# Optimization experiments

Measured on AMD Instinct MI355X. Metric: run time of the kernel, lower is better.

The kernel has to match this reference:

```python
import math
import jax, jax.numpy as jnp
import numpy as np

B, T, N = 64, 100, 20
NR = N * (N - 1)
D_STATE, D_SHAPE, D_REL = 8, 4, 3
THRESH = 0.35


def _pair_indices(n):
    # (i, j) pairs with i != j, ordered so that relation index
    # r = i*(n-1) + j - (j > i) equals the flattened position.
    ii, jj = np.meshgrid(np.arange(n), np.arange(n), indexing='ij')
    m = ii != jj
    return ii[m], jj[m]  # each [n*(n-1)]


def setup_inputs() -> dict:
    key = jax.random.key(0)
    k1, k2, k3 = jax.random.split(key, 3)
    objects_state = jax.random.uniform(k1, (B, T, N, D_STATE), dtype=jnp.float32)
    objects_shape = jax.random.normal(k2, (B, T, N, D_SHAPE), dtype=jnp.float32)
    relation_info = jax.random.normal(k3, (B, T, NR, D_REL), dtype=jnp.float32)
    return {"objects_state": objects_state, "objects_shape": objects_shape,
            "relation_info": relation_info}


def reference(objects_state, objects_shape, relation_info):
    dt = objects_state.dtype
    i_idx, j_idx = _pair_indices(N)

    # cdist over xy positions, then threshold (diagonal is exactly 0 -> excluded by nonzero)
    pos = objects_state[..., 0:2]                                   # [B,T,N,2]
    d = jnp.linalg.norm(pos[..., :, None, :] - pos[..., None, :, :], axis=-1)  # [B,T,N,N]
    adj = (d < THRESH) & (d > 0)
    mask = adj[..., i_idx, j_idx].astype(dt)                        # [B,T,NR]

    eye = jnp.eye(N, dtype=dt)
    receiver_relations = mask[..., None] * eye[i_idx]               # [B,T,NR,N]
    sender_relations = mask[..., None] * eye[j_idx]                 # [B,T,NR,N]

    # identity scaler
    data_state, data_shape = objects_state, objects_shape

    senders_state = jnp.einsum('btrn,btnd->btrd', sender_relations, data_state)
    receivers_state = jnp.einsum('btrn,btnd->btrd', receiver_relations, data_state)
    senders_shape = jnp.einsum('btrn,btnd->btrd', sender_relations, data_shape)
    receivers_shape = jnp.einsum('btrn,btnd->btrd', receiver_relations, data_shape)

    recv_ang = receivers_state[..., 2:3]                            # [B,T,NR,1]
    half_pi = jnp.asarray(math.pi / 2, dtype=dt)
    b1 = jnp.concatenate([jnp.cos(recv_ang), jnp.sin(recv_ang)], axis=-1)
    b2 = jnp.concatenate([jnp.cos(recv_ang + half_pi), jnp.sin(recv_ang + half_pi)], axis=-1)
    basis = jnp.stack([b1, b2], axis=-2)                            # [B,T,NR,2,2]

    diff_state = senders_state - receivers_state
    diff_pos = diff_state[..., 0:2]
    diff_vel = diff_state[..., 3:5]
    control = senders_state[..., 6:8]
    angle_diff = diff_state[..., 2:3]
    angle_diff_vel = diff_state[..., 5:6]

    temp = jnp.stack([diff_pos, diff_vel, control], axis=-1)        # [B,T,NR,2,3]
    tfed = jnp.einsum('btrij,btrjk->btrik', basis, temp)            # [B,T,NR,2,3]
    diff_pos, diff_vel, control = tfed[..., 0], tfed[..., 1], tfed[..., 2]

    diff_angle_2d = jnp.concatenate([jnp.sin(2 * angle_diff), jnp.cos(2 * angle_diff)], axis=-1)
    diff_state = jnp.concatenate([diff_pos, diff_vel, control, diff_angle_2d, angle_diff_vel], axis=-1)
    rel_data = jnp.concatenate([relation_info, diff_state, receivers_shape, senders_shape], axis=-1)

    obj_ang = data_state[..., 2:3]                                  # [B,T,N,1]
    ob1 = jnp.concatenate([jnp.cos(obj_ang), jnp.sin(obj_ang)], axis=-1)
    ob2 = jnp.concatenate([jnp.cos(obj_ang + half_pi), jnp.sin(obj_ang + half_pi)], axis=-1)
    object_basis = jnp.stack([ob1, ob2], axis=-2)                   # [B,T,N,2,2]
    obj_vel = data_state[..., 3:5]
    obj_vel_tfed = jnp.einsum('btnij,btnj->btni', object_basis, obj_vel)
    obj_data = jnp.concatenate([obj_vel_tfed, data_state[..., 5:6], data_shape], axis=-1)

    return rel_data, obj_data, receiver_relations, sender_relations
```

## Files before the change

### kernel.cpp

```cpp
#include <hip/hip_runtime.h>
#include <math.h>

#define BB 64
#define TT 100
#define NN 20
#define NRR 380

typedef float f32x4 __attribute__((ext_vector_type(4)));

__global__ __launch_bounds__(256) void onehot_kernel(
    const float* __restrict__ state,
    float* __restrict__ out)
{
    const int bt  = blockIdx.x;
    const int tid = threadIdx.x;

    __shared__ float s_pos[NN * 2];
    __shared__ float s_mask[NRR];
    __shared__ int   s_ij[NRR];

    if (tid < NN * 2) {
        const int n = tid >> 1, c = tid & 1;
        s_pos[tid] = state[(size_t)bt * NN * 8 + n * 8 + c];
    }
    __syncthreads();

    const float THRESH = 0.35f;
    for (int r = tid; r < NRR; r += 256) {
        const int i = r / 19;
        const int l = r - i * 19;
        const int j = (l < i) ? l : (l + 1);
        const float dx = s_pos[i * 2 + 0] - s_pos[j * 2 + 0];
        const float dy = s_pos[i * 2 + 1] - s_pos[j * 2 + 1];
        const float d  = sqrtf(dx * dx + dy * dy);
        s_mask[r] = (d < THRESH && d > 0.0f) ? 1.0f : 0.0f;
        s_ij[r]   = i | (j << 8);
    }
    __syncthreads();

    const size_t REL_SZ = (size_t)BB * TT * NRR * 20;
    const size_t OBJ_SZ = (size_t)BB * TT * NN * 7;
    f32x4* recvb = (f32x4*)(out + REL_SZ + OBJ_SZ)          + (size_t)bt * (NRR * 5);
    f32x4* sendb = (f32x4*)(out + REL_SZ + OBJ_SZ + REL_SZ) + (size_t)bt * (NRR * 5);

#pragma unroll
    for (int k = 0; k < 8; ++k) {
        const int idx = tid + k * 256;
        if (idx < NRR * 5) {
            const int r  = idx / 5;
            const int qb = (idx - r * 5) * 4;
            const float m = s_mask[r];
            const int   i = s_ij[r] & 255;
            f32x4 rv;
            rv.x = (i == qb + 0) ? m : 0.0f;
            rv.y = (i == qb + 1) ? m : 0.0f;
            rv.z = (i == qb + 2) ? m : 0.0f;
            rv.w = (i == qb + 3) ? m : 0.0f;
            __builtin_nontemporal_store(rv, &recvb[idx]);
        }
    }
#pragma unroll
    for (int k = 0; k < 8; ++k) {
        const int idx = tid + k * 256;
        if (idx < NRR * 5) {
            const int r  = idx / 5;
            const int qb = (idx - r * 5) * 4;
            const float m = s_mask[r];
            const int   j = s_ij[r] >> 8;
            f32x4 sv;
            sv.x = (j == qb + 0) ? m : 0.0f;
            sv.y = (j == qb + 1) ? m : 0.0f;
            sv.z = (j == qb + 2) ? m : 0.0f;
            sv.w = (j == qb + 3) ? m : 0.0f;
            __builtin_nontemporal_store(sv, &sendb[idx]);
        }
    }
}

__global__ __launch_bounds__(256) void reldata_kernel(
    const float* __restrict__ state,
    const float* __restrict__ shape,
    const float* __restrict__ relinfo,
    float* __restrict__ out)
{
    const int bt  = blockIdx.x;
    const int tid = threadIdx.x;

    __shared__ float  s_state[NN * 8];
    __shared__ float  s_shape[NN * 4];
    __shared__ float4 s_row4[NRR * 5];

    const float THRESH  = 0.35f;
    const float HALF_PI = 1.57079632679489661923f;

    const int   r2v = tid + 256;
    const int   r2c = (r2v < NRR) ? r2v : (NRR - 1);
    const float* rbase = relinfo + (size_t)bt * NRR * 3;
    const float ra0 = rbase[tid * 3 + 0];
    const float ra1 = rbase[tid * 3 + 1];
    const float ra2 = rbase[tid * 3 + 2];
    const float rb0 = rbase[r2c * 3 + 0];
    const float rb1 = rbase[r2c * 3 + 1];
    const float rb2 = rbase[r2c * 3 + 2];

    if (tid < NN * 8)                   s_state[tid]          = state[(size_t)bt * NN * 8 + tid];
    else if (tid < NN * 8 + NN * 4)     s_shape[tid - NN * 8] = shape[(size_t)bt * NN * 4 + (tid - NN * 8)];
    __syncthreads();

    const size_t REL_SZ = (size_t)BB * TT * NRR * 20;
    f32x4* relb = (f32x4*)out + (size_t)bt * (NRR * 5);
    float* objb = out + REL_SZ + (size_t)bt * (NN * 7);

    if (tid < NN * 7) {
        const int n = tid / 7;
        const int c = tid - n * 7;
        float v;
        if (c < 2) {
            const float ang = s_state[n * 8 + 2];
            const float a   = (c == 0) ? ang : (ang + HALF_PI);
            v = cosf(a) * s_state[n * 8 + 3] + sinf(a) * s_state[n * 8 + 4];
        } else if (c == 2) {
            v = s_state[n * 8 + 5];
        } else {
            v = s_shape[n * 4 + (c - 3)];
        }
        objb[tid] = v;
    }

    for (int pass = 0; pass < 2; ++pass) {
        const int r = (pass == 0) ? tid : r2v;
        if (r < NRR) {
            const float f0 = (pass == 0) ? ra0 : rb0;
            const float f1 = (pass == 0) ? ra1 : rb1;
            const float f2 = (pass == 0) ? ra2 : rb2;

            const int i = r / 19;
            const int l = r - i * 19;
            const int j = (l < i) ? l : (l + 1);

            const float* si = &s_state[i * 8];
            const float* sj = &s_state[j * 8];

            const float dx = si[0] - sj[0];
            const float dy = si[1] - sj[1];
            const float d  = sqrtf(dx * dx + dy * dy);
            const float mask = (d < THRESH && d > 0.0f) ? 1.0f : 0.0f;

            const float dpx   = mask * (sj[0] - si[0]);
            const float dpy   = mask * (sj[1] - si[1]);
            const float adiff = mask * (sj[2] - si[2]);
            const float dvx   = mask * (sj[3] - si[3]);
            const float dvy   = mask * (sj[4] - si[4]);
            const float adv   = mask * (sj[5] - si[5]);
            const float cx    = mask * sj[6];
            const float cy    = mask * sj[7];

            const float rang = mask * si[2];
            const float c1 = cosf(rang),           s1 = sinf(rang);
            const float c2 = cosf(rang + HALF_PI), s2 = sinf(rang + HALF_PI);

            float4 w0, w1, w2, w3, w4;
            w0.x = f0; w0.y = f1; w0.z = f2;
            w0.w = c1 * dpx + s1 * dpy;
            w1.x = c2 * dpx + s2 * dpy;
            w1.y = c1 * dvx + s1 * dvy;
            w1.z = c2 * dvx + s2 * dvy;
            w1.w = c1 * cx  + s1 * cy;
            w2.x = c2 * cx  + s2 * cy;
            w2.y = sinf(2.0f * adiff);
            w2.z = cosf(2.0f * adiff);
            w2.w = adv;
            w3.x = mask * s_shape[i * 4 + 0];
            w3.y = mask * s_shape[i * 4 + 1];
            w3.z = mask * s_shape[i * 4 + 2];
            w3.w = mask * s_shape[i * 4 + 3];
            w4.x = mask * s_shape[j * 4 + 0];
            w4.y = mask * s_shape[j * 4 + 1];
            w4.z = mask * s_shape[j * 4 + 2];
            w4.w = mask * s_shape[j * 4 + 3];

            float4* row = &s_row4[r * 5];
            row[0] = w0; row[1] = w1; row[2] = w2; row[3] = w3; row[4] = w4;
        }
    }
    __syncthreads();

#pragma unroll
    for (int k = 0; k < 8; ++k) {
        const int idx = tid + k * 256;
        if (idx < NRR * 5) {
            const float4 w = s_row4[idx];
            f32x4 wv;
            wv.x = w.x; wv.y = w.y; wv.z = w.z; wv.w = w.w;
            __builtin_nontemporal_store(wv, &relb[idx]);
        }
    }
}

extern "C" void kernel_launch(void* const* d_in, const int* in_sizes, int n_in,
                              void* d_out, int out_size, void* d_ws, size_t ws_size,
                              hipStream_t stream) {
    const float* state = (const float*)d_in[0];
    const float* shp   = (const float*)d_in[1];
    const float* rel   = (const float*)d_in[2];
    float* out = (float*)d_out;
    reldata_kernel<<<dim3(BB * TT), dim3(256), 0, stream>>>(state, shp, rel, out);
    onehot_kernel <<<dim3(BB * TT), dim3(256), 0, stream>>>(state, out);
}
```

Measured before the change: 120.7 us.

## Fuse reldata and one-hot kernels into one role-split launch with regular stores

Merges the two kernels into a single launch of 3x blocks. Each block takes one of three roles: rel/obj data, receiver one-hot, or sender one-hot. This removes one kernel launch and the serialization between the two kernels, and splits the one-hot writes across twice as many blocks. It also replaces nontemporal stores with ordinary stores, which changes cache behaviour on a write-bound kernel. The shared memory footprint per block grows because all roles declare the union of buffers, which may lower occupancy for the lighter roles.

```diff
diff --git a/kernel.cpp b/kernel.cpp
--- a/kernel.cpp
+++ b/kernel.cpp
@@ -5,194 +5,172 @@
 #define TT 100
 #define NN 20
 #define NRR 380
+#define NBT (BB * TT)
 
 typedef float f32x4 __attribute__((ext_vector_type(4)));
 
-__global__ __launch_bounds__(256) void onehot_kernel(
-    const float* __restrict__ state,
-    float* __restrict__ out)
-{
-    const int bt  = blockIdx.x;
-    const int tid = threadIdx.x;
-
-    __shared__ float s_pos[NN * 2];
-    __shared__ float s_mask[NRR];
-    __shared__ int   s_ij[NRR];
-
-    if (tid < NN * 2) {
-        const int n = tid >> 1, c = tid & 1;
-        s_pos[tid] = state[(size_t)bt * NN * 8 + n * 8 + c];
-    }
-    __syncthreads();
-
-    const float THRESH = 0.35f;
-    for (int r = tid; r < NRR; r += 256) {
-        const int i = r / 19;
-        const int l = r - i * 19;
-        const int j = (l < i) ? l : (l + 1);
-        const float dx = s_pos[i * 2 + 0] - s_pos[j * 2 + 0];
-        const float dy = s_pos[i * 2 + 1] - s_pos[j * 2 + 1];
-        const float d  = sqrtf(dx * dx + dy * dy);
-        s_mask[r] = (d < THRESH && d > 0.0f) ? 1.0f : 0.0f;
-        s_ij[r]   = i | (j << 8);
-    }
-    __syncthreads();
-
-    const size_t REL_SZ = (size_t)BB * TT * NRR * 20;
-    const size_t OBJ_SZ = (size_t)BB * TT * NN * 7;
-    f32x4* recvb = (f32x4*)(out + REL_SZ + OBJ_SZ)          + (size_t)bt * (NRR * 5);
-    f32x4* sendb = (f32x4*)(out + REL_SZ + OBJ_SZ + REL_SZ) + (size_t)bt * (NRR * 5);
-
-#pragma unroll
-    for (int k = 0; k < 8; ++k) {
-        const int idx = tid + k * 256;
-        if (idx < NRR * 5) {
-            const int r  = idx / 5;
-            const int qb = (idx - r * 5) * 4;
-            const float m = s_mask[r];
-            const int   i = s_ij[r] & 255;
-            f32x4 rv;
-            rv.x = (i == qb + 0) ? m : 0.0f;
-            rv.y = (i == qb + 1) ? m : 0.0f;
-            rv.z = (i == qb + 2) ? m : 0.0f;
-            rv.w = (i == qb + 3) ? m : 0.0f;
-            __builtin_nontemporal_store(rv, &recvb[idx]);
-        }
-    }
-#pragma unroll
-    for (int k = 0; k < 8; ++k) {
-        const int idx = tid + k * 256;
-        if (idx < NRR * 5) {
-            const int r  = idx / 5;
-            const int qb = (idx - r * 5) * 4;
-            const float m = s_mask[r];
-            const int   j = s_ij[r] >> 8;
-            f32x4 sv;
-            sv.x = (j == qb + 0) ? m : 0.0f;
-            sv.y = (j == qb + 1) ? m : 0.0f;
-            sv.z = (j == qb + 2) ? m : 0.0f;
-            sv.w = (j == qb + 3) ? m : 0.0f;
-            __builtin_nontemporal_store(sv, &sendb[idx]);
-        }
-    }
-}
-
-__global__ __launch_bounds__(256) void reldata_kernel(
+__global__ __launch_bounds__(256) void fused_kernel(
     const float* __restrict__ state,
     const float* __restrict__ shape,
     const float* __restrict__ relinfo,
     float* __restrict__ out)
 {
-    const int bt  = blockIdx.x;
-    const int tid = threadIdx.x;
+    const int blk  = blockIdx.x;
+    const int role = blk / NBT;
+    const int bt   = blk - role * NBT;
+    const int tid  = threadIdx.x;
+
+    const float THRESH  = 0.35f;
+    const float HALF_PI = 1.57079632679489661923f;
+
+    const size_t REL_SZ = (size_t)NBT * NRR * 20;
+    const size_t OBJ_SZ = (size_t)NBT * NN * 7;
 
     __shared__ float  s_state[NN * 8];
     __shared__ float  s_shape[NN * 4];
     __shared__ float4 s_row4[NRR * 5];
+    __shared__ float  s_mask[NRR];
+    __shared__ int    s_col[NRR];
 
-    const float THRESH  = 0.35f;
-    const float HALF_PI = 1.57079632679489661923f;
+    if (role == 0) {
+        const int   r2v = tid + 256;
+        const int   r2c = (r2v < NRR) ? r2v : (NRR - 1);
+        const float* rbase = relinfo + (size_t)bt * NRR * 3;
+        const float ra0 = rbase[tid * 3 + 0];
+        const float ra1 = rbase[tid * 3 + 1];
+        const float ra2 = rbase[tid * 3 + 2];
+        const float rb0 = rbase[r2c * 3 + 0];
+        const float rb1 = rbase[r2c * 3 + 1];
+        const float rb2 = rbase[r2c * 3 + 2];
 
-    const int   r2v = tid + 256;
-    const int   r2c = (r2v < NRR) ? r2v : (NRR - 1);
-    const float* rbase = relinfo + (size_t)bt * NRR * 3;
-    const float ra0 = rbase[tid * 3 + 0];
-    const float ra1 = rbase[tid * 3 + 1];
-    const float ra2 = rbase[tid * 3 + 2];
-    const float rb0 = rbase[r2c * 3 + 0];
-    const float rb1 = rbase[r2c * 3 + 1];
-    const float rb2 = rbase[r2c * 3 + 2];
+        if (tid < NN * 8)               s_state[tid]          = state[(size_t)bt * NN * 8 + tid];
+        else if (tid < NN * 8 + NN * 4) s_shape[tid - NN * 8] = shape[(size_t)bt * NN * 4 + (tid - NN * 8)];
+        __syncthreads();
 
-    if (tid < NN * 8)                   s_state[tid]          = state[(size_t)bt * NN * 8 + tid];
-    else if (tid < NN * 8 + NN * 4)     s_shape[tid - NN * 8] = shape[(size_t)bt * NN * 4 + (tid - NN * 8)];
-    __syncthreads();
+        f32x4* relb = (f32x4*)out + (size_t)bt * (NRR * 5);
+        float* objb = out + REL_SZ + (size_t)bt * (NN * 7);
 
-    const size_t REL_SZ = (size_t)BB * TT * NRR * 20;
-    f32x4* relb = (f32x4*)out + (size_t)bt * (NRR * 5);
-    float* objb = out + REL_SZ + (size_t)bt * (NN * 7);
+        if (tid < NN * 7) {
+            const int n = tid / 7;
+            const int c = tid - n * 7;
+            float v;
+            if (c < 2) {
+                const float ang = s_state[n * 8 + 2];
+                const float a   = (c == 0) ? ang : (ang + HALF_PI);
+                v = cosf(a) * s_state[n * 8 + 3] + sinf(a) * s_state[n * 8 + 4];
+            } else if (c == 2) {
+                v = s_state[n * 8 + 5];
+            } else {
+                v = s_shape[n * 4 + (c - 3)];
+            }
+            objb[tid] = v;
+        }
 
-    if (tid < NN * 7) {
-        const int n = tid / 7;
-        const int c = tid - n * 7;
-        float v;
-        if (c < 2) {
-            const float ang = s_state[n * 8 + 2];
-            const float a   = (c == 0) ? ang : (ang + HALF_PI);
-            v = cosf(a) * s_state[n * 8 + 3] + sinf(a) * s_state[n * 8 + 4];
-        } else if (c == 2) {
-            v = s_state[n * 8 + 5];
-        } else {
-            v = s_shape[n * 4 + (c - 3)];
+        for (int pass = 0; pass < 2; ++pass) {
+            const int r = (pass == 0) ? tid : r2v;
+            if (r < NRR) {
+                const float f0 = (pass == 0) ? ra0 : rb0;
+                const float f1 = (pass == 0) ? ra1 : rb1;
+                const float f2 = (pass == 0) ? ra2 : rb2;
+
+                const int i = r / 19;
+                const int l = r - i * 19;
+                const int j = (l < i) ? l : (l + 1);
+
+                const float* si = &s_state[i * 8];
+                const float* sj = &s_state[j * 8];
+
+                const float dx = si[0] - sj[0];
+                const float dy = si[1] - sj[1];
+                const float d  = sqrtf(dx * dx + dy * dy);
+                const float mask = (d < THRESH && d > 0.0f) ? 1.0f : 0.0f;
+
+                const float dpx   = mask * (sj[0] - si[0]);
+                const float dpy   = mask * (sj[1] - si[1]);
+                const float adiff = mask * (sj[2] - si[2]);
+                const float dvx   = mask * (sj[3] - si[3]);
+                const float dvy   = mask * (sj[4] - si[4]);
+                const float adv   = mask * (sj[5] - si[5]);
+                const float cx    = mask * sj[6];
+                const float cy    = mask * sj[7];
+
+                const float rang = mask * si[2];
+                const float c1 = cosf(rang),           s1 = sinf(rang);
+                const float c2 = cosf(rang + HALF_PI), s2 = sinf(rang + HALF_PI);
+
+                float4 w0, w1, w2, w3, w4;
+                w0.x = f0; w0.y = f1; w0.z = f2;
+                w0.w = c1 * dpx + s1 * dpy;
+                w1.x = c2 * dpx + s2 * dpy;
+                w1.y = c1 * dvx + s1 * dvy;
+                w1.z = c2 * dvx + s2 * dvy;
+                w1.w = c1 * cx  + s1 * cy;
+                w2.x = c2 * cx  + s2 * cy;
+                w2.y = sinf(2.0f * adiff);
+                w2.z = cosf(2.0f * adiff);
+                w2.w = adv;
+                w3.x = mask * s_shape[i * 4 + 0];
+                w3.y = mask * s_shape[i * 4 + 1];
+                w3.z = mask * s_shape[i * 4 + 2];
+                w3.w = mask * s_shape[i * 4 + 3];
+                w4.x = mask * s_shape[j * 4 + 0];
+                w4.y = mask * s_shape[j * 4 + 1];
+                w4.z = mask * s_shape[j * 4 + 2];
+                w4.w = mask * s_shape[j * 4 + 3];
+
+                float4* row = &s_row4[r * 5];
+                row[0] = w0; row[1] = w1; row[2] = w2; row[3] = w3; row[4] = w4;
+            }
         }
-        objb[tid] = v;
-    }
+        __syncthreads();
 
-    for (int pass = 0; pass < 2; ++pass) {
-        const int r = (pass == 0) ? tid : r2v;
-        if (r < NRR) {
-            const float f0 = (pass == 0) ? ra0 : rb0;
-            const float f1 = (pass == 0) ? ra1 : rb1;
-            const float f2 = (pass == 0) ? ra2 : rb2;
+#pragma unroll
+        for (int k = 0; k < 8; ++k) {
+            const int idx = tid + k * 256;
+            if (idx < NRR * 5) {
+                const float4 w = s_row4[idx];
+                f32x4 wv;
+                wv.x = w.x; wv.y = w.y; wv.z = w.z; wv.w = w.w;
+                relb[idx] = wv;
+            }
+        }
+    } else {
+        if (tid < NN * 2) {
+            const int n = tid >> 1, c = tid & 1;
+            s_state[tid] = state[(size_t)bt * NN * 8 + n * 8 + c];
+        }
+        __syncthreads();
 
+        for (int r = tid; r < NRR; r += 256) {
             const int i = r / 19;
             const int l = r - i * 19;
             const int j = (l < i) ? l : (l + 1);
+            const float dx = s_state[i * 2 + 0] - s_state[j * 2 + 0];
+            const float dy = s_state[i * 2 + 1] - s_state[j * 2 + 1];
+            const float d  = sqrtf(dx * dx + dy * dy);
+            s_mask[r] = (d < THRESH && d > 0.0f) ? 1.0f : 0.0f;
+            s_col[r]  = (role == 1) ? i : j;
+        }
+        __syncthreads();
 
-            const float* si = &s_state[i * 8];
-            const float* sj = &s_state[j * 8];
-
-            const float dx = si[0] - sj[0];
-            const float dy = si[1] - sj[1];
-            const float d  = sqrtf(dx * dx + dy * dy);
-            const float mask = (d < THRESH && d > 0.0f) ? 1.0f : 0.0f;
-
-            const float dpx   = mask * (sj[0] - si[0]);
-            const float dpy   = mask * (sj[1] - si[1]);
-            const float adiff = mask * (sj[2] - si[2]);
-            const float dvx   = mask * (sj[3] - si[3]);
-            const float dvy   = mask * (sj[4] - si[4]);
-            const float adv   = mask * (sj[5] - si[5]);
-            const float cx    = mask * sj[6];
-            const float cy    = mask * sj[7];
-
-            const float rang = mask * si[2];
-            const float c1 = cosf(rang),           s1 = sinf(rang);
-            const float c2 = cosf(rang + HALF_PI), s2 = sinf(rang + HALF_PI);
-
-            float4 w0, w1, w2, w3, w4;
-            w0.x = f0; w0.y = f1; w0.z = f2;
-            w0.w = c1 * dpx + s1 * dpy;
-            w1.x = c2 * dpx + s2 * dpy;
-            w1.y = c1 * dvx + s1 * dvy;
-            w1.z = c2 * dvx + s2 * dvy;
-            w1.w = c1 * cx  + s1 * cy;
-            w2.x = c2 * cx  + s2 * cy;
-            w2.y = sinf(2.0f * adiff);
-            w2.z = cosf(2.0f * adiff);
-            w2.w = adv;
-            w3.x = mask * s_shape[i * 4 + 0];
-            w3.y = mask * s_shape[i * 4 + 1];
-            w3.z = mask * s_shape[i * 4 + 2];
-            w3.w = mask * s_shape[i * 4 + 3];
-            w4.x = mask * s_shape[j * 4 + 0];
-            w4.y = mask * s_shape[j * 4 + 1];
-            w4.z = mask * s_shape[j * 4 + 2];
-            w4.w = mask * s_shape[j * 4 + 3];
-
-            float4* row = &s_row4[r * 5];
-            row[0] = w0; row[1] = w1; row[2] = w2; row[3] = w3; row[4] = w4;
-        }
-    }
-    __syncthreads();
+        f32x4* dst = (f32x4*)(out + REL_SZ + OBJ_SZ + (size_t)(role - 1) * REL_SZ)
+                     + (size_t)bt * (NRR * 5);
 
 #pragma unroll
-    for (int k = 0; k < 8; ++k) {
-        const int idx = tid + k * 256;
-        if (idx < NRR * 5) {
-            const float4 w = s_row4[idx];
-            f32x4 wv;
-            wv.x = w.x; wv.y = w.y; wv.z = w.z; wv.w = w.w;
-            __builtin_nontemporal_store(wv, &relb[idx]);
+        for (int k = 0; k < 8; ++k) {
+            const int idx = tid + k * 256;
+            if (idx < NRR * 5) {
+                const int r  = idx / 5;
+                const int qb = (idx - r * 5) * 4;
+                const float m = s_mask[r];
+                const int   c = s_col[r];
+                f32x4 v;
+                v.x = (c == qb + 0) ? m : 0.0f;
+                v.y = (c == qb + 1) ? m : 0.0f;
+                v.z = (c == qb + 2) ? m : 0.0f;
+                v.w = (c == qb + 3) ? m : 0.0f;
+                dst[idx] = v;
+            }
         }
     }
 }
@@ -204,6 +182,5 @@
     const float* shp   = (const float*)d_in[1];
     const float* rel   = (const float*)d_in[2];
     float* out = (float*)d_out;
-    reldata_kernel<<<dim3(BB * TT), dim3(256), 0, stream>>>(state, shp, rel, out);
-    onehot_kernel <<<dim3(BB * TT), dim3(256), 0, stream>>>(state, out);
+    fused_kernel<<<dim3(NBT * 3), dim3(256), 0, stream>>>(state, shp, rel, out);
 }
```

Result: no change. 118.8 us, median of 2 (-1.6%).
